# Kernel tuning notes

Hardware: AMD Instinct MI355X
Metric: run time of the kernel (lower is better)

The kernel has to match this reference:

```python
import jax, jax.numpy as jnp
import numpy as np

B, F0, D = 1024, 32, 32
HID = [128, 128, 128]


def setup_inputs() -> dict:
    key = jax.random.key(0)
    ks = jax.random.split(key, 4)
    inputs = jax.random.normal(ks[0], (B, F0, D), dtype=jnp.float32)
    # glorot-like init for conv filters, flattened to (F0*Fk, H)
    def glorot(k, fan_in, fan_out):
        lim = np.sqrt(6.0 / (fan_in + fan_out)).astype(np.float32)
        return jax.random.uniform(k, (fan_in, fan_out), dtype=jnp.float32, minval=-lim, maxval=lim)
    W0 = glorot(ks[1], F0 * F0, HID[0])
    W1 = glorot(ks[2], F0 * HID[0], HID[1])
    W2 = glorot(ks[3], F0 * HID[1], HID[2])
    b0 = jnp.zeros((HID[0],), dtype=jnp.float32)
    b1 = jnp.zeros((HID[1],), dtype=jnp.float32)
    b2 = jnp.zeros((HID[2],), dtype=jnp.float32)
    return {"inputs": inputs, "W0": W0, "W1": W1, "W2": W2,
            "b0": b0, "b1": b1, "b2": b2,
            "field_size": F0, "embedding_size": D}


def _cin_layer(x0, state, W, b):
    # x0: (B, F0, D), state: (B, Fk, D)
    bsz, f0, d = x0.shape
    fk = state.shape[1]
    # per-embedding-dim outer product; flatten (f0, fk) row-major to match
    # tf reshape of matmul(state_split_0, state_split_k^T)
    z = jnp.einsum('bfd,bgd->bdfg', x0, state).reshape(bsz, d, f0 * fk)
    h = z @ W + b  # (B, D, H); 1x1 conv1d == matmul over f0*fk
    # activation is linear (identity)
    return jnp.transpose(h, (0, 2, 1))  # (B, H, D)


def reference(inputs, W0, W1, W2, b0, b1, b2, field_size, embedding_size):
    x0 = inputs.reshape(-1, field_size, embedding_size)
    state = x0
    outputs = []
    for W, b in ((W0, b0), (W1, b1), (W2, b2)):
        fm = _cin_layer(x0, state, W, b)
        state = fm          # skip=False: state and output are the full map
        outputs.append(fm)
    # concat over field axis, sum over embedding dim -> (B, sum(H))
    return jnp.sum(jnp.concatenate(outputs, axis=1), axis=-1)
```

## Files before the change

### kernel.cpp

```cpp
#include <hip/hip_runtime.h>
#include <hip/hip_bf16.h>


typedef __attribute__((ext_vector_type(8))) short short8;
typedef __attribute__((ext_vector_type(8))) __bf16 bf16x8;
typedef __attribute__((ext_vector_type(16))) float f32x16;
typedef __attribute__((ext_vector_type(4))) unsigned short u16x4;

#define DEVINL static __device__ __forceinline__

DEVINL unsigned short f2bf_rne(float f) {
  unsigned int u = __builtin_bit_cast(unsigned int, f);
  unsigned int r = u + 0x7fffu + ((u >> 16) & 1u);
  return (unsigned short)(r >> 16);
}

template <typename V>
DEVINL auto mfma_32x32x16_bf16(V a, V b, f32x16 c, int)
    -> decltype(__builtin_amdgcn_mfma_f32_32x32x16_bf16(a, b, c, 0, 0, 0)) {
  return __builtin_amdgcn_mfma_f32_32x32x16_bf16(a, b, c, 0, 0, 0);
}
template <typename V>
DEVINL f32x16 mfma_32x32x16_bf16(V a, V b, f32x16 c, long) {
  return __builtin_amdgcn_mfma_f32_32x32x16_bf16(
      __builtin_bit_cast(bf16x8, a), __builtin_bit_cast(bf16x8, b), c, 0, 0, 0);
}
DEVINL f32x16 mfma_bf16(short8 a, short8 b, f32x16 c) {
  return mfma_32x32x16_bf16(a, b, c, 0);
}

__global__ void pack_w_kernel(const float* __restrict__ W0,
                              const float* __restrict__ W1,
                              const float* __restrict__ W2,
                              unsigned short* __restrict__ Wt) {
  __shared__ float tile[8][132];
  const int u = blockIdx.x;
  const float* W; int FK, f, kb, base;
  if (u < 128)      { W = W0; FK = 32;  f = u >> 2;         kb = u & 3;          base = 0; }
  else if (u < 640) { W = W1; FK = 128; f = (u - 128) >> 4; kb = (u - 128) & 15; base = 131072; }
  else              { W = W2; FK = 128; f = (u - 640) >> 4; kb = (u - 640) & 15; base = 655360; }
  const int t = threadIdx.x;
#pragma unroll
  for (int i = 0; i < 4; ++i) {
    const int e = t + i * 256;
    const int kk = e >> 7, h = e & 127;
    tile[kk][h] = W[(f * FK + kb * 8 + kk) * 128 + h];
  }
  __syncthreads();
  unsigned short* dst = Wt + base + f * (FK / 8) * 1024 + kb * 1024;
  const int h = t >> 1;
  const int j0 = (t & 1) * 4;
  u16x4 v;
  v.x = f2bf_rne(tile[j0 + 0][h]);
  v.y = f2bf_rne(tile[j0 + 1][h]);
  v.z = f2bf_rne(tile[j0 + 2][h]);
  v.w = f2bf_rne(tile[j0 + 3][h]);
  *(u16x4*)&dst[t * 4] = v;
}

template <int KQ, int STEPS, int LAYER>
DEVINL void run_layer(const unsigned short* __restrict__ WtL,
                      const float* __restrict__ bias,
                      const float* __restrict__ x0g,
                      float* __restrict__ outp, int outoff,
                      unsigned int* SB,
                      int wgb0, int mrow, int npair, int l31, int half) {
  __syncthreads();

  int4 sfr[2][KQ];
  const int rb = npair * 64;
#pragma unroll
  for (int nt = 0; nt < 2; ++nt) {
    const int r = rb + nt * 32 + l31;
#pragma unroll
    for (int kq = 0; kq < KQ; ++kq) {
      const int row0 = kq * 8 + half * 4;
      int4 v;
      v.x = (int)SB[(row0 + 0) * 128 + r];
      v.y = (int)SB[(row0 + 1) * 128 + r];
      v.z = (int)SB[(row0 + 2) * 128 + r];
      v.w = (int)SB[(row0 + 3) * 128 + r];
      sfr[nt][kq] = v;
    }
  }

  f32x16 zv;
#pragma unroll
  for (int e = 0; e < 16; ++e) zv[e] = 0.f;
  f32x16 outacc[2] = {zv, zv};

  const char* gb = (const char*)WtL +
                   (size_t)(half * 2048 + (mrow * 32 + l31) * 16);
  const int xb0 = (wgb0 + npair * 2 + 0) * 1024 + l31;
  const int xb1 = (wgb0 + npair * 2 + 1) * 1024 + l31;

  auto ldq = [&](short8* wv, int q) {
#pragma unroll
    for (int i = 0; i < 4; ++i)
      wv[i] = *(const short8*)(gb + (size_t)q * 16384 + i * 4096);
  };

  if constexpr (KQ == 8) {
    short8 w0[4], w1[4], w2[4], w3[4];
    float xc00 = x0g[xb0], xc01 = x0g[xb1];
    float xc10 = x0g[xb0 + 32], xc11 = x0g[xb1 + 32];
    ldq(w0, 0);
    ldq(w1, 1);
    __syncthreads();

    auto doFld = [&](const short8* qa, const short8* qb, float xs0, float xs1) {
      f32x16 Y0, Y1;
#pragma unroll
      for (int i = 0; i < 4; ++i) {
        const short8 s0 = __builtin_bit_cast(short8, sfr[0][i]);
        const short8 s1 = __builtin_bit_cast(short8, sfr[1][i]);
        Y0 = mfma_bf16(qa[i], s0, i == 0 ? zv : Y0);
        Y1 = mfma_bf16(qa[i], s1, i == 0 ? zv : Y1);
      }
#pragma unroll
      for (int i = 0; i < 4; ++i) {
        const short8 s0 = __builtin_bit_cast(short8, sfr[0][4 + i]);
        const short8 s1 = __builtin_bit_cast(short8, sfr[1][4 + i]);
        Y0 = mfma_bf16(qb[i], s0, Y0);
        Y1 = mfma_bf16(qb[i], s1, Y1);
      }
#pragma unroll
      for (int e = 0; e < 16; ++e) {
        outacc[0][e] += xs0 * Y0[e];
        outacc[1][e] += xs1 * Y1[e];
      }
    };

#pragma unroll 1
    for (int it = 0; it < 16; ++it) {
      const int f = 2 * it;
      float xn00 = xc00, xn01 = xc01, xn10 = xc10, xn11 = xc11;
      if (it < 15) {
        xn00 = x0g[xb0 + (f + 2) * 32]; xn01 = x0g[xb1 + (f + 2) * 32];
        xn10 = x0g[xb0 + (f + 3) * 32]; xn11 = x0g[xb1 + (f + 3) * 32];
      }
      ldq(w2, 4 * it + 2);
      ldq(w3, 4 * it + 3);
      doFld(w0, w1, xc00, xc01);
      if (it < 15) {
        ldq(w0, 4 * it + 4);
        ldq(w1, 4 * it + 5);
      }
      doFld(w2, w3, xc10, xc11);
      xc00 = xn00; xc01 = xn01; xc10 = xn10; xc11 = xn11;
    }
  } else {
    short8 wa[4], wb[4];
    float xa0 = x0g[xb0], xa1 = x0g[xb1];
    float xa2 = x0g[xb0 + 32], xa3 = x0g[xb1 + 32];
    ldq(wa, 0);
    __syncthreads();

    const short8 s00 = __builtin_bit_cast(short8, sfr[0][0]);
    const short8 s01 = __builtin_bit_cast(short8, sfr[0][1]);
    const short8 s10 = __builtin_bit_cast(short8, sfr[1][0]);
    const short8 s11 = __builtin_bit_cast(short8, sfr[1][1]);
    auto doQ = [&](const short8* wv, float x0a, float x1a, float x0b,
                   float x1b) {
      f32x16 Y0 = mfma_bf16(wv[0], s00, zv);
      Y0 = mfma_bf16(wv[1], s01, Y0);
      f32x16 Y1 = mfma_bf16(wv[0], s10, zv);
      Y1 = mfma_bf16(wv[1], s11, Y1);
#pragma unroll
      for (int e = 0; e < 16; ++e) {
        outacc[0][e] += x0a * Y0[e];
        outacc[1][e] += x1a * Y1[e];
      }
      Y0 = mfma_bf16(wv[2], s00, zv);
      Y0 = mfma_bf16(wv[3], s01, Y0);
      Y1 = mfma_bf16(wv[2], s10, zv);
      Y1 = mfma_bf16(wv[3], s11, Y1);
#pragma unroll
      for (int e = 0; e < 16; ++e) {
        outacc[0][e] += x0b * Y0[e];
        outacc[1][e] += x1b * Y1[e];
      }
    };

#pragma unroll 1
    for (int q2 = 0; q2 < 8; ++q2) {
      const int q = 2 * q2;
      const float xm0 = x0g[xb0 + (2 * q + 2) * 32];
      const float xm1 = x0g[xb1 + (2 * q + 2) * 32];
      const float xm2 = x0g[xb0 + (2 * q + 3) * 32];
      const float xm3 = x0g[xb1 + (2 * q + 3) * 32];
      ldq(wb, q + 1);
      float xn0 = xa0, xn1 = xa1, xn2 = xa2, xn3 = xa3;
      if (q2 < 7) {
        xn0 = x0g[xb0 + (2 * q + 4) * 32];
        xn1 = x0g[xb1 + (2 * q + 4) * 32];
        xn2 = x0g[xb0 + (2 * q + 5) * 32];
        xn3 = x0g[xb1 + (2 * q + 5) * 32];
      }
      doQ(wa, xa0, xa1, xa2, xa3);
      if (q2 < 7) ldq(wa, q + 2);
      doQ(wb, xm0, xm1, xm2, xm3);
      xa0 = xn0; xa1 = xn1; xa2 = xn2; xa3 = xn3;
    }
  }

  float bv[16];
#pragma unroll
  for (int e = 0; e < 16; ++e)
    bv[e] = bias[mrow * 32 + (e & 3) + 8 * (e >> 2) + 4 * half];

  if constexpr (LAYER < 2) {
#pragma unroll
    for (int nt = 0; nt < 2; ++nt) {
      const int r = rb + nt * 32 + l31;
#pragma unroll
      for (int g = 0; g < 4; ++g) {
        const int h2 = mrow * 16 + 4 * g + 2 * half;
        const float v0 = outacc[nt][4 * g + 0] + bv[4 * g + 0];
        const float v1 = outacc[nt][4 * g + 1] + bv[4 * g + 1];
        const float v2 = outacc[nt][4 * g + 2] + bv[4 * g + 2];
        const float v3 = outacc[nt][4 * g + 3] + bv[4 * g + 3];
        SB[h2 * 128 + r] =
            (unsigned)f2bf_rne(v0) | ((unsigned)f2bf_rne(v1) << 16);
        SB[(h2 + 1) * 128 + r] =
            (unsigned)f2bf_rne(v2) | ((unsigned)f2bf_rne(v3) << 16);
      }
    }
  }

#pragma unroll
  for (int nt = 0; nt < 2; ++nt) {
    float sv[16];
#pragma unroll
    for (int e = 0; e < 16; ++e) {
      float v = outacc[nt][e];
      v += __shfl_xor(v, 1);
      v += __shfl_xor(v, 2);
      v += __shfl_xor(v, 4);
      v += __shfl_xor(v, 8);
      v += __shfl_xor(v, 16);
      sv[e] = v + 32.0f * bv[e];
    }
    if (l31 == 0) {
      const int b = npair * 2 + nt;
#pragma unroll
      for (int g = 0; g < 4; ++g) {
        const int h = mrow * 32 + 8 * g + 4 * half;
        float4 o = {sv[4 * g + 0], sv[4 * g + 1], sv[4 * g + 2], sv[4 * g + 3]};
        *(float4*)&outp[b * 384 + outoff + h] = o;
      }
    }
  }
}

DEVINL void run_layer2_fast(const unsigned short* __restrict__ WtL,
                            const float* __restrict__ bias,
                            const float* __restrict__ x0g,
                            float* __restrict__ outp,
                            unsigned int* SB, int wgb0,
                            int w, int l31, int half, int tid) {
  __syncthreads();

  f32x16 zv;
#pragma unroll
  for (int e = 0; e < 16; ++e) zv[e] = 0.f;

  const int bw = w >> 1, gh = w & 1;
  short8 a1[2];
  {
    const float* xr = &x0g[(size_t)((wgb0 + bw) * 32 + l31) * 32];
#pragma unroll
    for (int kq = 0; kq < 2; ++kq) {
      const int d0 = kq * 16 + half * 8;
      union { short8 v; unsigned short u[8]; } t;
#pragma unroll
      for (int j = 0; j < 8; ++j) t.u[j] = f2bf_rne(xr[d0 + j]);
      a1[kq] = t.v;
    }
  }
  short8 bfr[2][2];
#pragma unroll
  for (int nt = 0; nt < 2; ++nt) {
    const int g = gh * 64 + nt * 32 + l31;
    const unsigned int* row = &SB[(g >> 1) * 128 + bw * 32];
    const int sh = (g & 1) * 16;
#pragma unroll
    for (int kq = 0; kq < 2; ++kq) {
      const int d0 = kq * 16 + half * 8;
      union { short8 v; unsigned short u[8]; } t;
#pragma unroll
      for (int j = 0; j < 8; ++j)
        t.u[j] = (unsigned short)(row[d0 + j] >> sh);
      bfr[nt][kq] = t.v;
    }
  }
  f32x16 ua[2];
#pragma unroll
  for (int nt = 0; nt < 2; ++nt) {
    ua[nt] = mfma_bf16(a1[0], bfr[nt][0], zv);
    ua[nt] = mfma_bf16(a1[1], bfr[nt][1], ua[nt]);
  }
  __syncthreads();

  unsigned short* U16 = (unsigned short*)SB;
#pragma unroll
  for (int nt = 0; nt < 2; ++nt) {
    const int g = gh * 64 + nt * 32 + l31;
#pragma unroll
    for (int reg = 0; reg < 16; ++reg) {
      const int f = (reg & 3) + 8 * (reg >> 2) + 4 * half;
      const int k = f * 128 + g;
      U16[(k >> 1) * 8 + bw * 2 + (k & 1)] = f2bf_rne(ua[nt][reg]);
    }
  }
  __syncthreads();

  const int mt = w & 3, kh = w >> 2;
  const char* gb = (const char*)WtL +
                   (size_t)(half * 2048 + (mt * 32 + l31) * 16);
  const int bl = l31 & 3;

  auto ldq2 = [&](short8* wv, int q) {
#pragma unroll
    for (int i = 0; i < 4; ++i)
      wv[i] = *(const short8*)(gb + (size_t)q * 16384 + i * 4096);
  };
  auto breadq = [&](short8* bv, int q) {
#pragma unroll
    for (int i = 0; i < 4; ++i) {
      const int row0 = (q * 4 + i) * 8 + half * 4;
      int4 v;
      v.x = (int)SB[(row0 + 0) * 4 + bl];
      v.y = (int)SB[(row0 + 1) * 4 + bl];
      v.z = (int)SB[(row0 + 2) * 4 + bl];
      v.w = (int)SB[(row0 + 3) * 4 + bl];
      bv[i] = __builtin_bit_cast(short8, v);
    }
  };

  f32x16 acc0 = zv, acc1 = zv;
  short8 qa[4], qb[4], Ba[4], Bb[4];
  const int q0 = kh * 32;
  ldq2(qa, q0);
  breadq(Ba, q0);
#pragma unroll 1
  for (int qq = 0; qq < 16; ++qq) {
    const int q = q0 + 2 * qq;
    ldq2(qb, q + 1);
    breadq(Bb, q + 1);
#pragma unroll
    for (int i = 0; i < 4; ++i) acc0 = mfma_bf16(qa[i], Ba[i], acc0);
    if (qq < 15) {
      ldq2(qa, q + 2);
      breadq(Ba, q + 2);
    }
#pragma unroll
    for (int i = 0; i < 4; ++i) acc1 = mfma_bf16(qb[i], Bb[i], acc1);
  }
#pragma unroll
  for (int e = 0; e < 16; ++e) acc0[e] += acc1[e];

  __syncthreads();

  float* P = (float*)SB;
  if (l31 < 4) {
#pragma unroll
    for (int reg = 0; reg < 16; ++reg) {
      const int h = mt * 32 + (reg & 3) + 8 * (reg >> 2) + 4 * half;
      P[(l31 * 128 + h) * 2 + kh] = acc0[reg];
    }
  }
  __syncthreads();
  {
    const int b = tid >> 7, h = tid & 127;
    const float v = P[tid * 2] + P[tid * 2 + 1] + 32.0f * bias[h];
    outp[b * 384 + 256 + h] = v;
  }
}

__global__ __launch_bounds__(512, 1) void cin_kernel(
    const float* __restrict__ x0g, const unsigned short* __restrict__ Wt,
    const float* __restrict__ b0, const float* __restrict__ b1,
    const float* __restrict__ b2, float* __restrict__ out) {
  __shared__ unsigned int SB[64 * 128];

  const int t = threadIdx.x;
  const int lane = t & 63;
  const int w = t >> 6;
  const int mrow = w & 3;
  const int npair = w >> 2;
  const int l31 = lane & 31, half = lane >> 5;
  const int wgb0 = blockIdx.x * 4;

#pragma unroll
  for (int s = 0; s < 4; ++s) {
    const int i = t + s * 512;
    const int r = i & 127, g2 = i >> 7;
    const float* p = &x0g[(wgb0 + (r >> 5)) * 1024 + (2 * g2) * 32 + (r & 31)];
    SB[g2 * 128 + r] =
        (unsigned)f2bf_rne(p[0]) | ((unsigned)f2bf_rne(p[32]) << 16);
  }

  float* outp = out + (size_t)wgb0 * 384;
  run_layer<2, 8, 0>(Wt, b0, x0g, outp, 0, SB, wgb0, mrow, npair, l31, half);
  run_layer<8, 32, 1>(Wt + 131072, b1, x0g, outp, 128, SB,
                      wgb0, mrow, npair, l31, half);
  run_layer2_fast(Wt + 655360, b2, x0g, outp, SB, wgb0, w, l31, half, t);
}

extern "C" void kernel_launch(void* const* d_in, const int* in_sizes, int n_in,
                              void* d_out, int out_size, void* d_ws, size_t ws_size,
                              hipStream_t stream) {
  (void)in_sizes; (void)n_in; (void)out_size; (void)ws_size;
  const float* x0 = (const float*)d_in[0];
  const float* W0 = (const float*)d_in[1];
  const float* W1 = (const float*)d_in[2];
  const float* W2 = (const float*)d_in[3];
  const float* b0 = (const float*)d_in[4];
  const float* b1 = (const float*)d_in[5];
  const float* b2 = (const float*)d_in[6];
  unsigned short* Wt = (unsigned short*)d_ws;

  pack_w_kernel<<<1152, 256, 0, stream>>>(W0, W1, W2, Wt);
  cin_kernel<<<256, 512, 0, stream>>>(x0, Wt, b0, b1, b2, (float*)d_out);
}
```

Measured before the change: 133.4 us.

## Use 1024-thread blocks with one batch row per wave group

Doubles the block size from 8 to 16 waves. In layers 0 and 1 each wave now handles a single batch element instead of two, and in layer 2 the K split is widened from 2 to 4 partial sums. The aim is more waves in flight to hide global weight-load latency and MFMA dependency chains, with less register pressure per wave. The cost is that each weight fragment loaded from global memory is reused across half as many batch rows, so per-block weight traffic doubles, and layer 2 now needs a 4-way partial-sum reduction through shared memory.

```diff
diff --git a/kernel.cpp b/kernel.cpp
--- a/kernel.cpp
+++ b/kernel.cpp
@@ -58,41 +58,36 @@
   *(u16x4*)&dst[t * 4] = v;
 }
 
-template <int KQ, int STEPS, int LAYER>
+template <int KQ, int LAYER>
 DEVINL void run_layer(const unsigned short* __restrict__ WtL,
                       const float* __restrict__ bias,
                       const float* __restrict__ x0g,
                       float* __restrict__ outp, int outoff,
                       unsigned int* SB,
-                      int wgb0, int mrow, int npair, int l31, int half) {
-  __syncthreads();
-
-  int4 sfr[2][KQ];
-  const int rb = npair * 64;
-#pragma unroll
-  for (int nt = 0; nt < 2; ++nt) {
-    const int r = rb + nt * 32 + l31;
-#pragma unroll
-    for (int kq = 0; kq < KQ; ++kq) {
-      const int row0 = kq * 8 + half * 4;
-      int4 v;
-      v.x = (int)SB[(row0 + 0) * 128 + r];
-      v.y = (int)SB[(row0 + 1) * 128 + r];
-      v.z = (int)SB[(row0 + 2) * 128 + r];
-      v.w = (int)SB[(row0 + 3) * 128 + r];
-      sfr[nt][kq] = v;
-    }
+                      int wgb0, int mrow, int bw, int l31, int half) {
+  __syncthreads();
+
+  int4 sfr[KQ];
+  const int r = bw * 32 + l31;
+#pragma unroll
+  for (int kq = 0; kq < KQ; ++kq) {
+    const int row0 = kq * 8 + half * 4;
+    int4 v;
+    v.x = (int)SB[(row0 + 0) * 128 + r];
+    v.y = (int)SB[(row0 + 1) * 128 + r];
+    v.z = (int)SB[(row0 + 2) * 128 + r];
+    v.w = (int)SB[(row0 + 3) * 128 + r];
+    sfr[kq] = v;
   }
 
   f32x16 zv;
 #pragma unroll
   for (int e = 0; e < 16; ++e) zv[e] = 0.f;
-  f32x16 outacc[2] = {zv, zv};
+  f32x16 outacc = zv;
 
   const char* gb = (const char*)WtL +
                    (size_t)(half * 2048 + (mrow * 32 + l31) * 16);
-  const int xb0 = (wgb0 + npair * 2 + 0) * 1024 + l31;
-  const int xb1 = (wgb0 + npair * 2 + 1) * 1024 + l31;
+  const int xb = (wgb0 + bw) * 1024 + l31;
 
   auto ldq = [&](short8* wv, int q) {
 #pragma unroll
@@ -100,107 +95,68 @@
       wv[i] = *(const short8*)(gb + (size_t)q * 16384 + i * 4096);
   };
 
+  short8 wa[4], wb[4];
+
   if constexpr (KQ == 8) {
-    short8 w0[4], w1[4], w2[4], w3[4];
-    float xc00 = x0g[xb0], xc01 = x0g[xb1];
-    float xc10 = x0g[xb0 + 32], xc11 = x0g[xb1 + 32];
-    ldq(w0, 0);
-    ldq(w1, 1);
+    float xs = x0g[xb];
+    ldq(wa, 0);
+    ldq(wb, 1);
     __syncthreads();
 
-    auto doFld = [&](const short8* qa, const short8* qb, float xs0, float xs1) {
-      f32x16 Y0, Y1;
+#pragma unroll 1
+    for (int f = 0; f < 32; ++f) {
+      float xn = xs;
+      if (f < 31) xn = x0g[xb + (f + 1) * 32];
+      f32x16 Y;
 #pragma unroll
       for (int i = 0; i < 4; ++i) {
-        const short8 s0 = __builtin_bit_cast(short8, sfr[0][i]);
-        const short8 s1 = __builtin_bit_cast(short8, sfr[1][i]);
-        Y0 = mfma_bf16(qa[i], s0, i == 0 ? zv : Y0);
-        Y1 = mfma_bf16(qa[i], s1, i == 0 ? zv : Y1);
+        const short8 s = __builtin_bit_cast(short8, sfr[i]);
+        Y = mfma_bf16(wa[i], s, i == 0 ? zv : Y);
       }
+      if (f < 31) ldq(wa, 2 * f + 2);
 #pragma unroll
       for (int i = 0; i < 4; ++i) {
-        const short8 s0 = __builtin_bit_cast(short8, sfr[0][4 + i]);
-        const short8 s1 = __builtin_bit_cast(short8, sfr[1][4 + i]);
-        Y0 = mfma_bf16(qb[i], s0, Y0);
-        Y1 = mfma_bf16(qb[i], s1, Y1);
+        const short8 s = __builtin_bit_cast(short8, sfr[4 + i]);
+        Y = mfma_bf16(wb[i], s, Y);
       }
-#pragma unroll
-      for (int e = 0; e < 16; ++e) {
-        outacc[0][e] += xs0 * Y0[e];
-        outacc[1][e] += xs1 * Y1[e];
-      }
-    };
-
-#pragma unroll 1
-    for (int it = 0; it < 16; ++it) {
-      const int f = 2 * it;
-      float xn00 = xc00, xn01 = xc01, xn10 = xc10, xn11 = xc11;
-      if (it < 15) {
-        xn00 = x0g[xb0 + (f + 2) * 32]; xn01 = x0g[xb1 + (f + 2) * 32];
-        xn10 = x0g[xb0 + (f + 3) * 32]; xn11 = x0g[xb1 + (f + 3) * 32];
-      }
-      ldq(w2, 4 * it + 2);
-      ldq(w3, 4 * it + 3);
-      doFld(w0, w1, xc00, xc01);
-      if (it < 15) {
-        ldq(w0, 4 * it + 4);
-        ldq(w1, 4 * it + 5);
-      }
-      doFld(w2, w3, xc10, xc11);
-      xc00 = xn00; xc01 = xn01; xc10 = xn10; xc11 = xn11;
+      if (f < 31) ldq(wb, 2 * f + 3);
+#pragma unroll
+      for (int e = 0; e < 16; ++e) outacc[e] += xs * Y[e];
+      xs = xn;
     }
   } else {
-    short8 wa[4], wb[4];
-    float xa0 = x0g[xb0], xa1 = x0g[xb1];
-    float xa2 = x0g[xb0 + 32], xa3 = x0g[xb1 + 32];
+    float xa0 = x0g[xb], xa1 = x0g[xb + 32];
     ldq(wa, 0);
     __syncthreads();
 
-    const short8 s00 = __builtin_bit_cast(short8, sfr[0][0]);
-    const short8 s01 = __builtin_bit_cast(short8, sfr[0][1]);
-    const short8 s10 = __builtin_bit_cast(short8, sfr[1][0]);
-    const short8 s11 = __builtin_bit_cast(short8, sfr[1][1]);
-    auto doQ = [&](const short8* wv, float x0a, float x1a, float x0b,
-                   float x1b) {
-      f32x16 Y0 = mfma_bf16(wv[0], s00, zv);
-      Y0 = mfma_bf16(wv[1], s01, Y0);
-      f32x16 Y1 = mfma_bf16(wv[0], s10, zv);
-      Y1 = mfma_bf16(wv[1], s11, Y1);
-#pragma unroll
-      for (int e = 0; e < 16; ++e) {
-        outacc[0][e] += x0a * Y0[e];
-        outacc[1][e] += x1a * Y1[e];
-      }
-      Y0 = mfma_bf16(wv[2], s00, zv);
-      Y0 = mfma_bf16(wv[3], s01, Y0);
-      Y1 = mfma_bf16(wv[2], s10, zv);
-      Y1 = mfma_bf16(wv[3], s11, Y1);
-#pragma unroll
-      for (int e = 0; e < 16; ++e) {
-        outacc[0][e] += x0b * Y0[e];
-        outacc[1][e] += x1b * Y1[e];
-      }
+    const short8 s0 = __builtin_bit_cast(short8, sfr[0]);
+    const short8 s1 = __builtin_bit_cast(short8, sfr[KQ - 1]);
+    auto doQ = [&](const short8* wv, float xA, float xB) {
+      f32x16 Y = mfma_bf16(wv[0], s0, zv);
+      Y = mfma_bf16(wv[1], s1, Y);
+#pragma unroll
+      for (int e = 0; e < 16; ++e) outacc[e] += xA * Y[e];
+      Y = mfma_bf16(wv[2], s0, zv);
+      Y = mfma_bf16(wv[3], s1, Y);
+#pragma unroll
+      for (int e = 0; e < 16; ++e) outacc[e] += xB * Y[e];
     };
 
 #pragma unroll 1
     for (int q2 = 0; q2 < 8; ++q2) {
       const int q = 2 * q2;
-      const float xm0 = x0g[xb0 + (2 * q + 2) * 32];
-      const float xm1 = x0g[xb1 + (2 * q + 2) * 32];
-      const float xm2 = x0g[xb0 + (2 * q + 3) * 32];
-      const float xm3 = x0g[xb1 + (2 * q + 3) * 32];
+      const float xm0 = x0g[xb + (2 * q + 2) * 32];
+      const float xm1 = x0g[xb + (2 * q + 3) * 32];
       ldq(wb, q + 1);
-      float xn0 = xa0, xn1 = xa1, xn2 = xa2, xn3 = xa3;
+      float xn0 = xa0, xn1 = xa1;
       if (q2 < 7) {
-        xn0 = x0g[xb0 + (2 * q + 4) * 32];
-        xn1 = x0g[xb1 + (2 * q + 4) * 32];
-        xn2 = x0g[xb0 + (2 * q + 5) * 32];
-        xn3 = x0g[xb1 + (2 * q + 5) * 32];
+        xn0 = x0g[xb + (2 * q + 4) * 32];
+        xn1 = x0g[xb + (2 * q + 5) * 32];
       }
-      doQ(wa, xa0, xa1, xa2, xa3);
+      doQ(wa, xa0, xa1);
       if (q2 < 7) ldq(wa, q + 2);
-      doQ(wb, xm0, xm1, xm2, xm3);
-      xa0 = xn0; xa1 = xn1; xa2 = xn2; xa3 = xn3;
+      doQ(wb, xm0, xm1);
+      xa0 = xn0; xa1 = xn1;
     }
   }
 
@@ -211,44 +167,35 @@
 
   if constexpr (LAYER < 2) {
 #pragma unroll
-    for (int nt = 0; nt < 2; ++nt) {
-      const int r = rb + nt * 32 + l31;
-#pragma unroll
-      for (int g = 0; g < 4; ++g) {
-        const int h2 = mrow * 16 + 4 * g + 2 * half;
-        const float v0 = outacc[nt][4 * g + 0] + bv[4 * g + 0];
-        const float v1 = outacc[nt][4 * g + 1] + bv[4 * g + 1];
-        const float v2 = outacc[nt][4 * g + 2] + bv[4 * g + 2];
-        const float v3 = outacc[nt][4 * g + 3] + bv[4 * g + 3];
-        SB[h2 * 128 + r] =
-            (unsigned)f2bf_rne(v0) | ((unsigned)f2bf_rne(v1) << 16);
-        SB[(h2 + 1) * 128 + r] =
-            (unsigned)f2bf_rne(v2) | ((unsigned)f2bf_rne(v3) << 16);
-      }
-    }
-  }
-
-#pragma unroll
-  for (int nt = 0; nt < 2; ++nt) {
-    float sv[16];
-#pragma unroll
-    for (int e = 0; e < 16; ++e) {
-      float v = outacc[nt][e];
-      v += __shfl_xor(v, 1);
-      v += __shfl_xor(v, 2);
-      v += __shfl_xor(v, 4);
-      v += __shfl_xor(v, 8);
-      v += __shfl_xor(v, 16);
-      sv[e] = v + 32.0f * bv[e];
-    }
-    if (l31 == 0) {
-      const int b = npair * 2 + nt;
-#pragma unroll
-      for (int g = 0; g < 4; ++g) {
-        const int h = mrow * 32 + 8 * g + 4 * half;
-        float4 o = {sv[4 * g + 0], sv[4 * g + 1], sv[4 * g + 2], sv[4 * g + 3]};
-        *(float4*)&outp[b * 384 + outoff + h] = o;
-      }
+    for (int g = 0; g < 4; ++g) {
+      const int h2 = mrow * 16 + 4 * g + 2 * half;
+      const float v0 = outacc[4 * g + 0] + bv[4 * g + 0];
+      const float v1 = outacc[4 * g + 1] + bv[4 * g + 1];
+      const float v2 = outacc[4 * g + 2] + bv[4 * g + 2];
+      const float v3 = outacc[4 * g + 3] + bv[4 * g + 3];
+      SB[h2 * 128 + r] = (unsigned)f2bf_rne(v0) | ((unsigned)f2bf_rne(v1) << 16);
+      SB[(h2 + 1) * 128 + r] =
+          (unsigned)f2bf_rne(v2) | ((unsigned)f2bf_rne(v3) << 16);
+    }
+  }
+
+  float sv[16];
+#pragma unroll
+  for (int e = 0; e < 16; ++e) {
+    float v = outacc[e];
+    v += __shfl_xor(v, 1);
+    v += __shfl_xor(v, 2);
+    v += __shfl_xor(v, 4);
+    v += __shfl_xor(v, 8);
+    v += __shfl_xor(v, 16);
+    sv[e] = v + 32.0f * bv[e];
+  }
+  if (l31 == 0) {
+#pragma unroll
+    for (int g = 0; g < 4; ++g) {
+      const int h = mrow * 32 + 8 * g + 4 * half;
+      float4 o = {sv[4 * g + 0], sv[4 * g + 1], sv[4 * g + 2], sv[4 * g + 3]};
+      *(float4*)&outp[bw * 384 + outoff + h] = o;
     }
   }
 }
@@ -265,10 +212,10 @@
 #pragma unroll
   for (int e = 0; e < 16; ++e) zv[e] = 0.f;
 
-  const int bw = w >> 1, gh = w & 1;
+  const int bw = w >> 2, gt = w & 3;
   short8 a1[2];
   {
-    const float* xr = &x0g[(size_t)((wgb0 + bw) * 32 + l31) * 32];
+    const float* xr = &x0g[(size_t)(wgb0 + bw) * 1024 + l31 * 32];
 #pragma unroll
     for (int kq = 0; kq < 2; ++kq) {
       const int d0 = kq * 16 + half * 8;
@@ -278,10 +225,9 @@
       a1[kq] = t.v;
     }
   }
-  short8 bfr[2][2];
-#pragma unroll
-  for (int nt = 0; nt < 2; ++nt) {
-    const int g = gh * 64 + nt * 32 + l31;
+  short8 bfr[2];
+  {
+    const int g = gt * 32 + l31;
     const unsigned int* row = &SB[(g >> 1) * 128 + bw * 32];
     const int sh = (g & 1) * 16;
 #pragma unroll
@@ -291,26 +237,21 @@
 #pragma unroll
       for (int j = 0; j < 8; ++j)
         t.u[j] = (unsigned short)(row[d0 + j] >> sh);
-      bfr[nt][kq] = t.v;
-    }
-  }
-  f32x16 ua[2];
-#pragma unroll
-  for (int nt = 0; nt < 2; ++nt) {
-    ua[nt] = mfma_bf16(a1[0], bfr[nt][0], zv);
-    ua[nt] = mfma_bf16(a1[1], bfr[nt][1], ua[nt]);
-  }
+      bfr[kq] = t.v;
+    }
+  }
+  f32x16 ua = mfma_bf16(a1[0], bfr[0], zv);
+  ua = mfma_bf16(a1[1], bfr[1], ua);
   __syncthreads();
 
   unsigned short* U16 = (unsigned short*)SB;
-#pragma unroll
-  for (int nt = 0; nt < 2; ++nt) {
-    const int g = gh * 64 + nt * 32 + l31;
+  {
+    const int g = gt * 32 + l31;
 #pragma unroll
     for (int reg = 0; reg < 16; ++reg) {
       const int f = (reg & 3) + 8 * (reg >> 2) + 4 * half;
       const int k = f * 128 + g;
-      U16[(k >> 1) * 8 + bw * 2 + (k & 1)] = f2bf_rne(ua[nt][reg]);
+      U16[(k >> 1) * 8 + bw * 2 + (k & 1)] = f2bf_rne(ua[reg]);
     }
   }
   __syncthreads();
@@ -340,17 +281,17 @@
 
   f32x16 acc0 = zv, acc1 = zv;
   short8 qa[4], qb[4], Ba[4], Bb[4];
-  const int q0 = kh * 32;
+  const int q0 = kh * 16;
   ldq2(qa, q0);
   breadq(Ba, q0);
 #pragma unroll 1
-  for (int qq = 0; qq < 16; ++qq) {
+  for (int qq = 0; qq < 8; ++qq) {
     const int q = q0 + 2 * qq;
     ldq2(qb, q + 1);
     breadq(Bb, q + 1);
 #pragma unroll
     for (int i = 0; i < 4; ++i) acc0 = mfma_bf16(qa[i], Ba[i], acc0);
-    if (qq < 15) {
+    if (qq < 7) {
       ldq2(qa, q + 2);
       breadq(Ba, q + 2);
     }
@@ -367,18 +308,19 @@
 #pragma unroll
     for (int reg = 0; reg < 16; ++reg) {
       const int h = mt * 32 + (reg & 3) + 8 * (reg >> 2) + 4 * half;
-      P[(l31 * 128 + h) * 2 + kh] = acc0[reg];
-    }
-  }
-  __syncthreads();
-  {
+      P[(l31 * 128 + h) * 4 + kh] = acc0[reg];
+    }
+  }
+  __syncthreads();
+  if (tid < 512) {
     const int b = tid >> 7, h = tid & 127;
-    const float v = P[tid * 2] + P[tid * 2 + 1] + 32.0f * bias[h];
+    const float v = P[tid * 4] + P[tid * 4 + 1] + P[tid * 4 + 2] +
+                    P[tid * 4 + 3] + 32.0f * bias[h];
     outp[b * 384 + 256 + h] = v;
   }
 }
 
-__global__ __launch_bounds__(512, 1) void cin_kernel(
+__global__ __launch_bounds__(1024, 1) void cin_kernel(
     const float* __restrict__ x0g, const unsigned short* __restrict__ Wt,
     const float* __restrict__ b0, const float* __restrict__ b1,
     const float* __restrict__ b2, float* __restrict__ out) {
@@ -388,13 +330,13 @@
   const int lane = t & 63;
   const int w = t >> 6;
   const int mrow = w & 3;
-  const int npair = w >> 2;
+  const int bw = w >> 2;
   const int l31 = lane & 31, half = lane >> 5;
   const int wgb0 = blockIdx.x * 4;
 
 #pragma unroll
-  for (int s = 0; s < 4; ++s) {
-    const int i = t + s * 512;
+  for (int s = 0; s < 2; ++s) {
+    const int i = t + s * 1024;
     const int r = i & 127, g2 = i >> 7;
     const float* p = &x0g[(wgb0 + (r >> 5)) * 1024 + (2 * g2) * 32 + (r & 31)];
     SB[g2 * 128 + r] =
@@ -402,9 +344,9 @@
   }
 
   float* outp = out + (size_t)wgb0 * 384;
-  run_layer<2, 8, 0>(Wt, b0, x0g, outp, 0, SB, wgb0, mrow, npair, l31, half);
-  run_layer<8, 32, 1>(Wt + 131072, b1, x0g, outp, 128, SB,
-                      wgb0, mrow, npair, l31, half);
+  run_layer<2, 0>(Wt, b0, x0g, outp, 0, SB, wgb0, mrow, bw, l31, half);
+  run_layer<8, 1>(Wt + 131072, b1, x0g, outp, 128, SB,
+                  wgb0, mrow, bw, l31, half);
   run_layer2_fast(Wt + 655360, b2, x0g, outp, SB, wgb0, w, l31, half, t);
 }
 
@@ -422,5 +364,5 @@
   unsigned short* Wt = (unsigned short*)d_ws;
 
   pack_w_kernel<<<1152, 256, 0, stream>>>(W0, W1, W2, Wt);
-  cin_kernel<<<256, 512, 0, stream>>>(x0, Wt, b0, b1, b2, (float*)d_out);
-}
+  cin_kernel<<<256, 1024, 0, stream>>>(x0, Wt, b0, b1, b2, (float*)d_out);
+}
```

New measurement: 143.6 us. 7.6% more time.
